# Optimization experiments

Hardware: AMD Instinct MI355X
Metric: run time of the kernel (lower is better)

Reference implementation:

```python
import jax, jax.numpy as jnp
import numpy as np

NUM_Q, NUM_C, E = 12000, 1000, 256
B, S, MC = 32, 200, 4
H = E  # hidden_size == emb_size


def _mlp(x, lin_w, lin_b, out_w, out_b):
    # MLP with n_layer=1: relu(Linear) then output Linear (dropout is identity in eval)
    x = jax.nn.relu(x @ lin_w.T + lin_b)
    return x @ out_w.T + out_b


def _lstm(x, w_ih, w_hh, b_ih, b_hh):
    # torch nn.LSTM(batch_first) semantics, gate order i,f,g,o
    def step(carry, xt):
        h, cs = carry
        gates = xt @ w_ih.T + b_ih + h @ w_hh.T + b_hh
        i, f, g, o = jnp.split(gates, 4, axis=-1)
        cs = jax.nn.sigmoid(f) * cs + jax.nn.sigmoid(i) * jnp.tanh(g)
        h = jax.nn.sigmoid(o) * jnp.tanh(cs)
        return (h, cs), h
    b = x.shape[0]
    init = (jnp.zeros((b, H), x.dtype), jnp.zeros((b, H), x.dtype))
    _, hs = jax.lax.scan(step, init, jnp.swapaxes(x, 0, 1))
    return jnp.swapaxes(hs, 0, 1)


def _avg_fusion_concepts(y_concept, cshft):
    # gather-average over concept ids (equivalent to one_hot*mul*sum in the torch code)
    mask = (cshft != -1)
    idx = jnp.where(mask, cshft, 0)
    gathered = jnp.take_along_axis(y_concept, idx, axis=-1) * mask  # [B,S-1,MC]
    cnt = mask.sum(-1)
    return gathered.sum(-1) / jnp.maximum(cnt, 1)


def _avg_skill_emb(c, concept_emb):
    # QueEmb.get_avg_skill_emb: zero row prepended, -1 padding -> index 0
    cat = jnp.concatenate([jnp.zeros((1, E), concept_emb.dtype), concept_emb], axis=0)
    rc = c + 1
    s = cat[rc].sum(axis=-2)  # [B,S,E]
    n = jnp.maximum((rc != 0).sum(axis=-1), 1)
    return s / n[..., None]


def setup_inputs() -> dict:
    key = jax.random.key(0)
    ks = jax.random.split(key, 24)
    f = jnp.float32
    def lin(k, out_d, in_d):
        bound = 1.0 / np.sqrt(in_d)
        k1, k2 = jax.random.split(k)
        return (jax.random.uniform(k1, (out_d, in_d), f, -bound, bound),
                jax.random.uniform(k2, (out_d,), f, -bound, bound))
    qn_lw, qn_lb = lin(ks[0], 3 * H, 3 * H)
    qn_ow, qn_ob = lin(ks[1], 1, 3 * H)
    cn_lw, cn_lb = lin(ks[2], 3 * H, 3 * H)
    cn_ow, cn_ob = lin(ks[3], NUM_C, 3 * H)
    qa_lw, qa_lb = lin(ks[4], H, H)
    qa_ow, qa_ob = lin(ks[5], NUM_Q, H)
    ca_lw, ca_lb = lin(ks[6], H, H)
    ca_ow, ca_ob = lin(ks[7], NUM_C, H)
    w_ih, b_ih = lin(ks[8], 4 * H, 4 * E)
    w_hh, b_hh = lin(ks[9], 4 * H, H)
    return {
        'q': jax.random.randint(ks[10], (B, S), 0, NUM_Q),
        'c': jax.random.randint(ks[11], (B, S, MC), 0, NUM_C),
        'r': jax.random.randint(ks[12], (B, S), 0, 2),
        'qshft': jax.random.randint(ks[13], (B, S - 1), 0, NUM_Q),
        'cshft': jax.random.randint(ks[14], (B, S - 1, MC), 0, NUM_C),
        'que_emb': jax.random.normal(ks[15], (NUM_Q, E), f) * 0.02,
        'concept_emb': jax.random.normal(ks[16], (NUM_C, E), f) * 0.02,
        'w_ih': w_ih, 'w_hh': w_hh, 'b_ih': b_ih, 'b_hh': b_hh,
        'qn_lw': qn_lw, 'qn_lb': qn_lb, 'qn_ow': qn_ow, 'qn_ob': qn_ob,
        'cn_lw': cn_lw, 'cn_lb': cn_lb, 'cn_ow': cn_ow, 'cn_ob': cn_ob,
        'qa_lw': qa_lw, 'qa_lb': qa_lb, 'qa_ow': qa_ow, 'qa_ob': qa_ob,
        'ca_lw': ca_lw, 'ca_lb': ca_lb, 'ca_ow': ca_ow, 'ca_ob': ca_ob,
    }


def reference(q, c, r, qshft, cshft, que_emb, concept_emb, w_ih, w_hh, b_ih, b_hh,
              qn_lw, qn_lb, qn_ow, qn_ob, cn_lw, cn_lb, cn_ow, cn_ob,
              qa_lw, qa_lb, qa_ow, qa_ob, ca_lw, ca_lb, ca_ow, ca_ob):
    emb_q = que_emb[q]                               # [B,S,E]
    emb_c = _avg_skill_emb(c, concept_emb)           # [B,S,E]
    emb_qc = jnp.concatenate([emb_q, emb_c], -1)     # [B,S,2E]
    rf = r.astype(emb_qc.dtype)[..., None]
    emb_qca = jnp.concatenate([emb_qc * (1 - rf), emb_qc * rf], -1)  # [B,S,4E]

    emb_qc_shift = emb_qc[:, 1:]
    emb_qca_current = emb_qca[:, :-1]
    h = _lstm(emb_qca_current, w_ih, w_hh, b_ih, b_hh)  # [B,S-1,H]  (dropout: eval)
    h_next = jnp.concatenate([emb_qc_shift, h], -1)     # [B,S-1,3H]

    y_question_next = jax.nn.sigmoid(_mlp(h_next, qn_lw, qn_lb, qn_ow, qn_ob)).squeeze(-1)
    y_concept_next = jax.nn.sigmoid(_mlp(h_next, cn_lw, cn_lb, cn_ow, cn_ob))   # [B,S-1,num_c]
    y_question_all = jax.nn.sigmoid(_mlp(h, qa_lw, qa_lb, qa_ow, qa_ob))        # [B,S-1,num_q]
    y_concept_all = jax.nn.sigmoid(_mlp(h, ca_lw, ca_lb, ca_ow, ca_ob))         # [B,S-1,num_c]

    y_concept_next = _avg_fusion_concepts(y_concept_next, cshft)
    y_question_all = jnp.take_along_axis(y_question_all, qshft[..., None], axis=-1).squeeze(-1)
    y_concept_all = _avg_fusion_concepts(y_concept_all, cshft)
    return (y_question_next, y_concept_next, y_question_all, y_concept_all)
```

## Files before the change

### kernel.cpp

```cpp
#include <hip/hip_runtime.h>
#include <hip/hip_bf16.h>

typedef __hip_bfloat16 bf16;
typedef __attribute__((ext_vector_type(8))) short short8;
typedef __attribute__((ext_vector_type(4))) short short4v;
typedef __attribute__((ext_vector_type(4))) float float4v;

#define MFMA16(a,b,c) __builtin_amdgcn_mfma_f32_16x16x32_bf16((a),(b),(c),0,0,0)

#define NB 32
#define NS 200
#define NT 199
#define NBT (NB*NT)
#define HSTR 272

__device__ __forceinline__ float bf2f(bf16 x){ return __bfloat162float(x); }
__device__ __forceinline__ bf16 f2bf(float x){ return __float2bfloat16(x); }
__device__ __forceinline__ float rcp_(float x){ return __builtin_amdgcn_rcpf(x); }
__device__ __forceinline__ float sigmoidf_(float x){ return rcp_(1.0f+__expf(-x)); }
__device__ __forceinline__ float tanhf_(float x){ return 1.0f - 2.0f*rcp_(__expf(2.0f*x)+1.0f); }

union BU { bf16 b; unsigned short u; };
__device__ __forceinline__ unsigned short b2u(bf16 x){ BU t; t.b = x; return t.u; }
__device__ __forceinline__ float u2f(unsigned short x){ BU t; t.u = x; return bf2f(t.b); }

template<typename T>
__device__ __forceinline__ float ldf(const T* p, size_t i){
  if constexpr (sizeof(T) == 4) return p[i]; else return bf2f(p[i]);
}

__device__ __forceinline__ float wave_reduce(float v){
  #pragma unroll
  for (int o=32;o>0;o>>=1) v += __shfl_xor(v, o, 64);
  return v;
}

__device__ __forceinline__ void burn(int iters){
  float x = 1.0f;
  for (int i=0;i<iters;i++)
    x = __builtin_fmaf(x, 1.0000001f, 1.0e-9f);
  asm volatile("" :: "v"(x));
}

__device__ __forceinline__ int poll_xready_rlx(int* xchunk, int lane){
  int tgt = (lane < 25) ? ((lane == 24) ? 7 : 8) : 0;
  int v = 0;
  if (lane < 25)
    v = __hip_atomic_load(&xchunk[lane], __ATOMIC_RELAXED, __HIP_MEMORY_SCOPE_AGENT);
  unsigned long long full = __ballot(v >= tgt);
  unsigned long long notfull = ~full;
  int firstbad = (notfull == 0ULL) ? 64 : (__ffsll((unsigned long long)notfull) - 1);
  int rdy = firstbad * 8;
  return (rdy > NT) ? NT : rdy;
}

__global__ void k_detect(const unsigned short* qe, int* flag){
  int big = 0;
  for (int j = threadIdx.x; j < 128; j += 64){
    int ex = (qe[j] >> 7) & 0xFF;
    if (ex >= 128) big = 1;
  }
  unsigned long long m = __ballot(big);
  if (threadIdx.x == 0) flag[0] = (__popcll(m) >= 2) ? 1 : 0;
}

__global__ void k_sentinel(void* out, int n, float v, const int* flag){
  int i = blockIdx.x*256 + threadIdx.x;
  if (i < n){ if (flag[0]) ((float*)out)[i] = v; else ((bf16*)out)[i] = f2bf(v); }
}

__global__ __launch_bounds__(1024) void k_cvt(
    const void* s0, const void* s1, const void* s2, const void* s3,
    const void* s4, const void* s5, const void* s6, const void* s7,
    bf16* out, const int* flag){
  size_t i = (size_t)blockIdx.x*1024 + threadIdx.x;
  const size_t sz[8] = {1048576,262144,589824,589824,65536,65536,4096,4096};
  const void* sp[8] = {s0,s1,s2,s3,s4,s5,s6,s7};
  size_t off = i; int s = 0;
  while (s < 8 && off >= sz[s]){ off -= sz[s]; s++; }
  if (s >= 8) return;
  if (flag[0]) out[i] = f2bf(((const float*)sp[s])[off]);
  else         out[i] = ((const bf16*)sp[s])[off];
}

template<typename T>
__device__ __forceinline__ void embed_body(const int* q, const int* c,
    const T* que_emb, const T* concept_emb, bf16* emb_qc){
  int p = blockIdx.x;
  int e = threadIdx.x;
  int qi = q[p];
  emb_qc[(size_t)p*512 + e] = f2bf(ldf(que_emb, (size_t)qi*256 + e));
  float s = 0.f; int cnt = 0;
  #pragma unroll
  for (int m=0;m<4;m++){
    int ci = c[p*4+m];
    if (ci >= 0){ cnt++; s += ldf(concept_emb, (size_t)ci*256 + e); }
  }
  s /= (float)(cnt > 0 ? cnt : 1);
  emb_qc[(size_t)p*512 + 256 + e] = f2bf(s);
}
__global__ __launch_bounds__(256) void k_embed(const int* q, const int* c,
    const void* qe, const void* ce, bf16* emb_qc, const int* flag, int* cnt){
  if (blockIdx.x == 0 && threadIdx.x < 32) cnt[threadIdx.x] = 0;
  if (flag[0]) embed_body<float>(q, c, (const float*)qe, (const float*)ce, emb_qc);
  else         embed_body<bf16 >(q, c, (const bf16*)qe,  (const bf16*)ce,  emb_qc);
}

__device__ void gemm_x_unit(int t, int ny, int ltid, unsigned short* xs,
    const bf16* E, const int* r, const bf16* W, const bf16* bc1, const bf16* bc2, bf16* Xp){
  int lane = ltid & 63, wv = ltid >> 6;
  int col = lane & 15, quad = lane >> 4, kq = quad*8;
  const bf16* e0 = E + (size_t)(col*NS + t)*512;
  const bf16* e1 = E + (size_t)((col+16)*NS + t)*512;
  int rv0 = r[col*NS + t], rv1 = r[(col+16)*NS + t];
  int n_base = ny*256 + wv*64;
  const bf16* w0 = W + (size_t)(n_base + col)*1024 + kq;
  short8 z8 = {};
  float4v acc[2][4] = {};
  for (int k0 = 0; k0 < 1024; k0 += 32){
    bool lo = (k0 < 512);
    short8 a0 = *(const short8*)(e0 + (k0 & 511) + kq);
    short8 a1 = *(const short8*)(e1 + (k0 & 511) + kq);
    a0 = (lo == (rv0 == 0)) ? a0 : z8;
    a1 = (lo == (rv1 == 0)) ? a1 : z8;
    short8 bb[4];
    #pragma unroll
    for (int ni=0;ni<4;ni++) bb[ni] = *(const short8*)(w0 + (size_t)ni*16*1024 + k0);
    #pragma unroll
    for (int ni=0;ni<4;ni++){
      acc[0][ni] = MFMA16(a0, bb[ni], acc[0][ni]);
      acc[1][ni] = MFMA16(a1, bb[ni], acc[1][ni]);
    }
  }
  #pragma unroll
  for (int ni=0;ni<4;ni++){
    int n = n_base + ni*16 + col;
    float bs = bf2f(bc1[n]) + bf2f(bc2[n]);
    int nloc = wv*64 + ni*16 + col;
    #pragma unroll
    for (int mi=0;mi<2;mi++)
      #pragma unroll
      for (int reg=0;reg<4;reg++)
        xs[nloc*40 + mi*16 + quad*4 + reg] = b2u(f2bf(acc[mi][ni][reg] + bs));
  }
  __syncthreads();
  int nloc = ltid;
  size_t n = (size_t)ny*256 + nloc;
  short8 v0 = *(const short8*)&xs[nloc*40 + 0];
  short8 v1 = *(const short8*)&xs[nloc*40 + 8];
  short8 v2 = *(const short8*)&xs[nloc*40 + 16];
  short8 v3 = *(const short8*)&xs[nloc*40 + 24];
  bf16* base = Xp + (size_t)t*2*16384 + n*16;
  *(short8*)(base)             = v0;
  *(short8*)(base + 8)         = v1;
  *(short8*)(base + 16384)     = v2;
  *(short8*)(base + 16384 + 8) = v3;
}

__device__ void lstm_role(const bf16* Xp, const bf16* Whh, bf16* Hg,
                          unsigned short* smem, int* cnt){
  int* xchunk = cnt;
  int* hprog  = cnt + 25;
  unsigned short* wlds = smem;
  unsigned short* hbuf = smem + 65536;

  int lane = threadIdx.x & 63, w = threadIdx.x >> 6;
  int col = lane & 15, quad = lane >> 4, kq = quad*8;
  int b0 = blockIdx.x*16;

  for (int i = threadIdx.x; i < 16*HSTR; i += 512) hbuf[i] = 0;

  short8 bfrag[4][8];
  #pragma unroll
  for (int tix=0; tix<4; tix++){
    int g = tix >> 1, ct = tix & 1;
    int nb = g*256 + w*32 + ct*16;
    #pragma unroll
    for (int ks=0; ks<8; ks++)
      bfrag[tix][ks] = *(const volatile short8*)(Whh + (size_t)(nb + col)*256 + ks*32 + kq);
  }
  short8 wofrag[2][8];
  #pragma unroll
  for (int j=0; j<2; j++){
    int nb = 3*256 + w*32 + j*16;
    #pragma unroll
    for (int ks=0; ks<8; ks++)
      wofrag[j][ks] = *(const volatile short8*)(Whh + (size_t)(nb + col)*256 + ks*32 + kq);
  }
  #pragma unroll
  for (int j=0; j<2; j++){
    int nb = 2*256 + w*32 + j*16;
    #pragma unroll
    for (int ks=0; ks<8; ks++){
      short8 v = *(const short8*)(Whh + (size_t)(nb + col)*256 + ks*32 + kq);
      *(short8*)&wlds[(((w*2+j)*8 + ks)*64 + lane)*8] = v;
    }
  }
  __syncthreads();

  float cs[2][4] = {};
  short4v xq[8], xqn[8];

  int ready = 0;
  while (ready < 1){
    int p = poll_xready_rlx(xchunk, lane);
    if (p > ready){
      __builtin_amdgcn_fence(__ATOMIC_ACQUIRE, "agent");
      ready = p;
    } else __builtin_amdgcn_s_sleep(16);
  }
  {
    const bf16* xb = Xp + (size_t)blockIdx.x*16384 + quad*4;
    #pragma unroll
    for (int g=0; g<4; g++)
      #pragma unroll
      for (int ct=0; ct<2; ct++)
        xq[g*2+ct] = *(const short4v*)(xb + (size_t)(g*256 + w*32 + ct*16 + col)*16);
  }

  for (int t=0; t<NT; t++){
    int tn = (t+1 < NT) ? t+1 : t;
    while (ready < tn+1){
      int p = poll_xready_rlx(xchunk, lane);
      if (p > ready){
        __builtin_amdgcn_fence(__ATOMIC_ACQUIRE, "agent");
        ready = p;
      } else __builtin_amdgcn_s_sleep(16);
    }
    const bf16* xbn = Xp + ((size_t)tn*2 + blockIdx.x)*16384 + quad*4;
    #pragma unroll
    for (int g=0; g<4; g++)
      #pragma unroll
      for (int ct=0; ct<2; ct++)
        xqn[g*2+ct] = *(const short4v*)(xbn + (size_t)(g*256 + w*32 + ct*16 + col)*16);

    float4v acc[8];
    #pragma unroll
    for (int j=0; j<8; j++)
      #pragma unroll
      for (int rg=0; rg<4; rg++)
        acc[j][rg] = u2f((unsigned short)xq[j][rg]);

    const unsigned short* hrow = &hbuf[(t&1)*(16*HSTR) + col*HSTR + kq];
    #pragma unroll
    for (int ks=0; ks<8; ks++){
      short8 af = *(const short8*)(hrow + ks*32);
      #pragma unroll
      for (int tix=0; tix<4; tix++) acc[tix] = MFMA16(af, bfrag[tix][ks], acc[tix]);
      #pragma unroll
      for (int j=0; j<2; j++){
        short8 lw = *(const short8*)&wlds[(((w*2+j)*8 + ks)*64 + lane)*8];
        acc[4+j] = MFMA16(af, lw, acc[4+j]);
      }
      acc[6] = MFMA16(af, wofrag[0][ks], acc[6]);
      acc[7] = MFMA16(af, wofrag[1][ks], acc[7]);
    }

    unsigned short* hw = &hbuf[((t+1)&1)*(16*HSTR)];
    #pragma unroll
    for (int ct=0; ct<2; ct++){
      int hc = w*32 + ct*16 + col;
      #pragma unroll
      for (int reg=0; reg<4; reg++){
        float iv = sigmoidf_(acc[0+ct][reg]);
        float fv = sigmoidf_(acc[2+ct][reg]);
        float gv = tanhf_   (acc[4+ct][reg]);
        float ov = sigmoidf_(acc[6+ct][reg]);
        float cc = fv*cs[ct][reg] + iv*gv;
        cs[ct][reg] = cc;
        hw[(quad*4+reg)*HSTR + hc] = b2u(f2bf(ov*tanhf_(cc)));
      }
    }
    #pragma unroll
    for (int i=0;i<8;i++) xq[i] = xqn[i];
    __syncthreads();
    if (((t & 1) == 0) && threadIdx.x == ((((unsigned)t >> 1) & 7) << 6))
      __hip_atomic_store(&hprog[blockIdx.x], t, __ATOMIC_RELEASE, __HIP_MEMORY_SCOPE_AGENT);
    {
      int ri = threadIdx.x >> 5, ci2 = threadIdx.x & 31;
      short8 v = *(const short8*)&hbuf[((t+1)&1)*(16*HSTR) + ri*HSTR + ci2*8];
      *(short8*)(Hg + ((size_t)t*NB + b0 + ri)*256 + ci2*8) = v;
    }
  }
  __syncthreads();
  if (threadIdx.x == 0)
    __hip_atomic_store(&hprog[blockIdx.x], NT, __ATOMIC_RELEASE, __HIP_MEMORY_SCOPE_AGENT);
}

#define HPAD 776
#define SPAD 264
template<typename T>
__device__ void head_pair(int t0, int tid, unsigned short* hsb, unsigned short* hss,
    const bf16* E, const bf16* Hg,
    const bf16* qn_w, const bf16* cn_w, const bf16* qa_w, const bf16* ca_w,
    const T* qn_lb, const T* qn_ow, const T* qn_ob,
    const T* cn_lb, const T* cn_ow, const T* cn_ob,
    const T* qa_lb, const T* qa_ow, const T* qa_ob,
    const T* ca_lb, const T* ca_ow, const T* ca_ob,
    const int* qshft, const int* cshft, void* out, int isf32){
  int hf = tid >> 8, ltid = tid & 255;
  int lane = ltid & 63, wv = ltid >> 6;
  int col = lane & 15, quad = lane >> 4, kq = quad*8;
  const bf16* h0 = Hg + ((size_t)t0*NB + col)*256;
  const bf16* h1 = Hg + ((size_t)t0*NB + col + 16)*256;
  const bf16* e0 = E + ((size_t)col*NS + t0 + 1)*512;
  const bf16* e1 = E + ((size_t)(col+16)*NS + t0 + 1)*512;

  for (int hd=0; hd<2; hd++){
    if (hf == 0){
      const bf16* W = hd ? cn_w : qn_w;
      const T*   Bb = hd ? cn_lb : qn_lb;
      const bf16* wb = W + (size_t)(wv*192 + col)*768 + kq;
      float4v acc[2][12] = {};
      for (int k0 = 0; k0 < 768; k0 += 32){
        short8 a0 = (k0 < 512) ? *(const short8*)(e0 + k0 + kq)
                               : *(const short8*)(h0 + (k0-512) + kq);
        short8 a1 = (k0 < 512) ? *(const short8*)(e1 + k0 + kq)
                               : *(const short8*)(h1 + (k0-512) + kq);
        #pragma unroll
        for (int ni=0; ni<12; ni++){
          short8 bv = *(const short8*)(wb + (size_t)ni*16*768 + k0);
          acc[0][ni] = MFMA16(a0, bv, acc[0][ni]);
          acc[1][ni] = MFMA16(a1, bv, acc[1][ni]);
        }
      }
      #pragma unroll
      for (int ni=0; ni<12; ni++){
        int n = wv*192 + ni*16 + col;
        float bs = ldf(Bb, n);
        #pragma unroll
        for (int mi=0; mi<2; mi++)
          #pragma unroll
          for (int reg=0; reg<4; reg++){
            int rl = mi*16 + quad*4 + reg;
            hsb[rl*HPAD + n] = b2u(f2bf(fmaxf(acc[mi][ni][reg] + bs, 0.0f)));
          }
      }
    } else {
      const bf16* W = hd ? ca_w : qa_w;
      const T*   Bb = hd ? ca_lb : qa_lb;
      const bf16* wb = W + (size_t)(wv*64 + col)*256 + kq;
      float4v acc[2][4] = {};
      for (int k0 = 0; k0 < 256; k0 += 32){
        short8 av0 = *(const short8*)(h0 + k0 + kq);
        short8 av1 = *(const short8*)(h1 + k0 + kq);
        #pragma unroll
        for (int ni=0; ni<4; ni++){
          short8 bv = *(const short8*)(wb + (size_t)ni*16*256 + k0);
          acc[0][ni] = MFMA16(av0, bv, acc[0][ni]);
          acc[1][ni] = MFMA16(av1, bv, acc[1][ni]);
        }
      }
      #pragma unroll
      for (int ni=0; ni<4; ni++){
        int n = wv*64 + ni*16 + col;
        float bs = ldf(Bb, n);
        #pragma unroll
        for (int mi=0; mi<2; mi++)
          #pragma unroll
          for (int reg=0; reg<4; reg++){
            int rl = mi*16 + quad*4 + reg;
            hss[rl*SPAD + n] = b2u(f2bf(fmaxf(acc[mi][ni][reg] + bs, 0.0f)));
          }
      }
    }
    __syncthreads();
    if (hf == 0){
      for (int rr=0; rr<8; rr++){
        int rl = wv*8 + rr, p = rl*NT + t0;
        if (hd == 0){
          float d = 0.f;
          for (int i=lane; i<768; i+=64) d += u2f(hsb[rl*HPAD + i]) * ldf(qn_ow, i);
          d = wave_reduce(d);
          if (lane == 0){
            float v = sigmoidf_(d + ldf(qn_ob, 0));
            if (isf32) ((float*)out)[p] = v; else ((bf16*)out)[p] = f2bf(v);
          }
        } else {
          float sum = 0.f; int cnt = 0;
          #pragma unroll
          for (int m=0; m<4; m++){
            int cid = cshft[p*4+m];
            if (cid >= 0){
              cnt++;
              const T* ww = cn_ow + (size_t)cid*768;
              float d = 0.f;
              for (int i=lane; i<768; i+=64) d += u2f(hsb[rl*HPAD + i]) * ldf(ww, i);
              d = wave_reduce(d);
              sum += sigmoidf_(d + ldf(cn_ob, cid));
            }
          }
          if (lane == 0){
            float v = sum / (float)(cnt > 0 ? cnt : 1);
            if (isf32) ((float*)out)[NBT+p] = v; else ((bf16*)out)[NBT+p] = f2bf(v);
          }
        }
      }
    } else {
      for (int rr=0; rr<8; rr++){
        int rl = wv*8 + rr, p = rl*NT + t0;
        if (hd == 0){
          int qid = qshft[p];
          const T* ww = qa_ow + (size_t)qid*256;
          float d = 0.f;
          for (int i=lane; i<256; i+=64) d += u2f(hss[rl*SPAD + i]) * ldf(ww, i);
          d = wave_reduce(d);
          if (lane == 0){
            float v = sigmoidf_(d + ldf(qa_ob, qid));
            if (isf32) ((float*)out)[2*NBT+p] = v; else ((bf16*)out)[2*NBT+p] = f2bf(v);
          }
        } else {
          float sum = 0.f; int cnt = 0;
          #pragma unroll
          for (int m=0; m<4; m++){
            int cid = cshft[p*4+m];
            if (cid >= 0){
              cnt++;
              const T* ww = ca_ow + (size_t)cid*256;
              float d = 0.f;
              for (int i=lane; i<256; i+=64) d += u2f(hss[rl*SPAD + i]) * ldf(ww, i);
              d = wave_reduce(d);
              sum += sigmoidf_(d + ldf(ca_ob, cid));
            }
          }
          if (lane == 0){
            float v = sum / (float)(cnt > 0 ? cnt : 1);
            if (isf32) ((float*)out)[3*NBT+p] = v; else ((bf16*)out)[3*NBT+p] = f2bf(v);
          }
        }
      }
    }
    __syncthreads();
  }
}

__global__ __launch_bounds__(512)
__attribute__((amdgpu_waves_per_eu(2, 2)))
void k_fused(const bf16* E, const int* r, const bf16* wih, const bf16* bih, const bf16* bhh,
             bf16* Xp, const bf16* whh, bf16* Hg,
             const bf16* qn_w, const bf16* cn_w, const bf16* qa_w, const bf16* ca_w,
             const void* qn_lb, const void* qn_ow, const void* qn_ob,
             const void* cn_lb, const void* cn_ow, const void* cn_ob,
             const void* qa_lb, const void* qa_ow, const void* qa_ob,
             const void* ca_lb, const void* ca_ow, const void* ca_ob,
             const int* qshft, const int* cshft, void* out, const int* flag, int* cnt){
  extern __shared__ __align__(16) unsigned short smem[];
  int* xchunk = cnt;
  int* hprog  = cnt + 25;

  if (blockIdx.x < 2){
    lstm_role(Xp, whh, Hg, smem, cnt);
    return;
  }
  if ((blockIdx.x & 7) < 2){
    for (;;){
      int a = __hip_atomic_load(&hprog[0], __ATOMIC_RELAXED, __HIP_MEMORY_SCOPE_AGENT);
      int b = __hip_atomic_load(&hprog[1], __ATOMIC_RELAXED, __HIP_MEMORY_SCOPE_AGENT);
      if (a >= NT && b >= NT) break;
      burn(2048);
    }
    return;
  }

  int tid = threadIdx.x, hf = tid >> 8, ltid = tid & 255;
  int rank = blockIdx.x - 2*(blockIdx.x >> 3) - 2;
  int t1 = rank;
  int t2 = (rank < 49) ? rank + 150 : -1;
  volatile int* lflag = (volatile int*)(smem + 73728);

  for (int ti = 0; ti < 2; ti++){
    int t = (ti == 0) ? t1 : t2;
    if (t < 0) break;
    unsigned short* xs = smem + hf*(256*40);
    gemm_x_unit(t, hf,     ltid, xs, E, r, wih, bih, bhh, Xp);
    __syncthreads();
    gemm_x_unit(t, 2 + hf, ltid, xs, E, r, wih, bih, bhh, Xp);
    __syncthreads();
    if (tid == 0)
      __hip_atomic_fetch_add(&xchunk[t >> 3], 1, __ATOMIC_RELEASE, __HIP_MEMORY_SCOPE_AGENT);
  }

  unsigned short* hsb = smem;
  unsigned short* hss = smem + 32*HPAD;
  for (int ti = 0; ti < 2; ti++){
    int t0 = (ti == 0) ? t1 : t2;
    if (t0 < 0) break;
    if (tid == 0) *lflag = 0;
    __syncthreads();
    {
      int need = t0 + 1;
      for (;;){
        if (tid == 0){
          int a = __hip_atomic_load(&hprog[0], __ATOMIC_RELAXED, __HIP_MEMORY_SCOPE_AGENT);
          int b = __hip_atomic_load(&hprog[1], __ATOMIC_RELAXED, __HIP_MEMORY_SCOPE_AGENT);
          if (a >= need && b >= need){
            __builtin_amdgcn_fence(__ATOMIC_ACQUIRE, "agent");
            *lflag = 1;
          }
        }
        if (*lflag) break;
        burn(256);
      }
    }
    __syncthreads();

    if (flag[0])
      head_pair<float>(t0, tid, hsb, hss, E, Hg, qn_w, cn_w, qa_w, ca_w,
        (const float*)qn_lb, (const float*)qn_ow, (const float*)qn_ob,
        (const float*)cn_lb, (const float*)cn_ow, (const float*)cn_ob,
        (const float*)qa_lb, (const float*)qa_ow, (const float*)qa_ob,
        (const float*)ca_lb, (const float*)ca_ow, (const float*)ca_ob,
        qshft, cshft, out, 1);
    else
      head_pair<bf16>(t0, tid, hsb, hss, E, Hg, qn_w, cn_w, qa_w, ca_w,
        (const bf16*)qn_lb, (const bf16*)qn_ow, (const bf16*)qn_ob,
        (const bf16*)cn_lb, (const bf16*)cn_ow, (const bf16*)cn_ob,
        (const bf16*)qa_lb, (const bf16*)qa_ow, (const bf16*)qa_ob,
        (const bf16*)ca_lb, (const bf16*)ca_ow, (const bf16*)ca_ob,
        qshft, cshft, out, 0);
  }

  for (;;){
    int a = __hip_atomic_load(&hprog[0], __ATOMIC_RELAXED, __HIP_MEMORY_SCOPE_AGENT);
    int b = __hip_atomic_load(&hprog[1], __ATOMIC_RELAXED, __HIP_MEMORY_SCOPE_AGENT);
    if (a >= NT && b >= NT) break;
    burn(2048);
  }
}

extern "C" void kernel_launch(void* const* d_in, const int* in_sizes, int n_in,
                              void* d_out, int out_size, void* d_ws, size_t ws_size,
                              hipStream_t stream){
  const int*  q     = (const int*) d_in[0];
  const int*  c     = (const int*) d_in[1];
  const int*  r     = (const int*) d_in[2];
  const int*  qshft = (const int*) d_in[3];
  const int*  cshft = (const int*) d_in[4];
  const void* que_emb  = d_in[5];
  const void* conc_emb = d_in[6];
  const void* w_ih  = d_in[7];
  const void* w_hh  = d_in[8];
  const void* b_ih  = d_in[9];
  const void* b_hh  = d_in[10];
  const void* qn_lw = d_in[11];
  const void* qn_lb = d_in[12];
  const void* qn_ow = d_in[13];
  const void* qn_ob = d_in[14];
  const void* cn_lw = d_in[15];
  const void* cn_lb = d_in[16];
  const void* cn_ow = d_in[17];
  const void* cn_ob = d_in[18];
  const void* qa_lw = d_in[19];
  const void* qa_lb = d_in[20];
  const void* qa_ow = d_in[21];
  const void* qa_ob = d_in[22];
  const void* ca_lw = d_in[23];
  const void* ca_lb = d_in[24];
  const void* ca_ow = d_in[25];
  const void* ca_ob = d_in[26];

  const size_t OFF_FLAG = 0;
  const size_t OFF_EMB  = 256;
  const size_t OFF_XPT  = OFF_EMB + 6553600;
  const size_t OFF_HG   = OFF_XPT + 13041664;
  const size_t OFF_WC   = OFF_HG + 3260416;
  const size_t NEED     = OFF_WC + 5259264;

  char* ws = (char*)d_ws;
  int* flag = (int*)(ws + OFF_FLAG);
  int* cnt  = (int*)(ws + 64);

  k_detect<<<1, 64, 0, stream>>>((const unsigned short*)que_emb, flag);

  if (ws_size < NEED){
    k_sentinel<<<(out_size + 255)/256, 256, 0, stream>>>(d_out, out_size,
        (float)(ws_size >> 20), flag);
    return;
  }

  bf16* emb_qc = (bf16*)(ws + OFF_EMB);
  bf16* Xp     = (bf16*)(ws + OFF_XPT);
  bf16* Hg     = (bf16*)(ws + OFF_HG);
  bf16* Wc     = (bf16*)(ws + OFF_WC);
  bf16* wih_c  = Wc;
  bf16* whh_c  = Wc + 1048576;
  bf16* qnlw_c = Wc + 1310720;
  bf16* cnlw_c = Wc + 1900544;
  bf16* qalw_c = Wc + 2490368;
  bf16* calw_c = Wc + 2555904;
  bf16* bih_c  = Wc + 2621440;
  bf16* bhh_c  = Wc + 2625536;

  hipFuncSetAttribute((const void*)k_fused,
      hipFuncAttributeMaxDynamicSharedMemorySize, 148480);

  k_cvt<<<2568, 1024, 0, stream>>>(w_ih, w_hh, qn_lw, cn_lw, qa_lw, ca_lw,
      b_ih, b_hh, Wc, flag);
  k_embed<<<NB*NS, 256, 0, stream>>>(q, c, que_emb, conc_emb, emb_qc, flag, cnt);
  k_fused<<<201, 512, 148480, stream>>>(emb_qc, r, wih_c, bih_c, bhh_c, Xp, whh_c, Hg,
      qnlw_c, cnlw_c, qalw_c, calw_c,
      qn_lb, qn_ow, qn_ob, cn_lb, cn_ow, cn_ob,
      qa_lb, qa_ow, qa_ob, ca_lb, ca_ow, ca_ob,
      qshft, cshft, d_out, flag, cnt);
}
```

Before: 1.007 ms.

## Assign one timestep per block and replace burn-loop polling with s_sleep

Removes the earlier scheme where some blocks only spun as placeholders and each working block handled up to two timesteps. Now every non-LSTM block handles exactly one timestep: it computes its input-projection chunk, then waits on the LSTM progress counters using s_sleep instead of an FMA burn loop, then runs the output heads. The intent is to stop wasting CU issue slots on busy-wait ALU work and to spread head work across more blocks. This depends on the host launching one block per timestep, which is in the unseen launch code. If that launch grid was not updated, the change risks coverage gaps or co-residency deadlock, since blocks spin while waiting on other blocks.

```diff
diff --git a/kernel.cpp b/kernel.cpp
--- a/kernel.cpp
+++ b/kernel.cpp
@@ -33,13 +33,6 @@
   #pragma unroll
   for (int o=32;o>0;o>>=1) v += __shfl_xor(v, o, 64);
   return v;
-}
-
-__device__ __forceinline__ void burn(int iters){
-  float x = 1.0f;
-  for (int i=0;i<iters;i++)
-    x = __builtin_fmaf(x, 1.0000001f, 1.0e-9f);
-  asm volatile("" :: "v"(x));
 }
 
 __device__ __forceinline__ int poll_xready_rlx(int* xchunk, int lane){
@@ -452,80 +445,55 @@
     lstm_role(Xp, whh, Hg, smem, cnt);
     return;
   }
-  if ((blockIdx.x & 7) < 2){
-    for (;;){
-      int a = __hip_atomic_load(&hprog[0], __ATOMIC_RELAXED, __HIP_MEMORY_SCOPE_AGENT);
-      int b = __hip_atomic_load(&hprog[1], __ATOMIC_RELAXED, __HIP_MEMORY_SCOPE_AGENT);
-      if (a >= NT && b >= NT) break;
-      burn(2048);
-    }
-    return;
-  }
-
+
+  int t0  = blockIdx.x - 2;
   int tid = threadIdx.x, hf = tid >> 8, ltid = tid & 255;
-  int rank = blockIdx.x - 2*(blockIdx.x >> 3) - 2;
-  int t1 = rank;
-  int t2 = (rank < 49) ? rank + 150 : -1;
   volatile int* lflag = (volatile int*)(smem + 73728);
 
-  for (int ti = 0; ti < 2; ti++){
-    int t = (ti == 0) ? t1 : t2;
-    if (t < 0) break;
+  {
     unsigned short* xs = smem + hf*(256*40);
-    gemm_x_unit(t, hf,     ltid, xs, E, r, wih, bih, bhh, Xp);
+    gemm_x_unit(t0, hf,     ltid, xs, E, r, wih, bih, bhh, Xp);
     __syncthreads();
-    gemm_x_unit(t, 2 + hf, ltid, xs, E, r, wih, bih, bhh, Xp);
+    gemm_x_unit(t0, 2 + hf, ltid, xs, E, r, wih, bih, bhh, Xp);
+    if (tid == 0) *lflag = 0;
     __syncthreads();
     if (tid == 0)
-      __hip_atomic_fetch_add(&xchunk[t >> 3], 1, __ATOMIC_RELEASE, __HIP_MEMORY_SCOPE_AGENT);
-  }
+      __hip_atomic_fetch_add(&xchunk[t0 >> 3], 1, __ATOMIC_RELEASE, __HIP_MEMORY_SCOPE_AGENT);
+  }
+
+  {
+    int need = t0 + 1;
+    for (;;){
+      if (tid == 0){
+        int a = __hip_atomic_load(&hprog[0], __ATOMIC_RELAXED, __HIP_MEMORY_SCOPE_AGENT);
+        int b = __hip_atomic_load(&hprog[1], __ATOMIC_RELAXED, __HIP_MEMORY_SCOPE_AGENT);
+        if (a >= need && b >= need){
+          __builtin_amdgcn_fence(__ATOMIC_ACQUIRE, "agent");
+          *lflag = 1;
+        }
+      }
+      if (*lflag) break;
+      __builtin_amdgcn_s_sleep(32);
+    }
+  }
+  __syncthreads();
 
   unsigned short* hsb = smem;
   unsigned short* hss = smem + 32*HPAD;
-  for (int ti = 0; ti < 2; ti++){
-    int t0 = (ti == 0) ? t1 : t2;
-    if (t0 < 0) break;
-    if (tid == 0) *lflag = 0;
-    __syncthreads();
-    {
-      int need = t0 + 1;
-      for (;;){
-        if (tid == 0){
-          int a = __hip_atomic_load(&hprog[0], __ATOMIC_RELAXED, __HIP_MEMORY_SCOPE_AGENT);
-          int b = __hip_atomic_load(&hprog[1], __ATOMIC_RELAXED, __HIP_MEMORY_SCOPE_AGENT);
-          if (a >= need && b >= need){
-            __builtin_amdgcn_fence(__ATOMIC_ACQUIRE, "agent");
-            *lflag = 1;
-          }
-        }
-        if (*lflag) break;
-        burn(256);
-      }
-    }
-    __syncthreads();
-
-    if (flag[0])
-      head_pair<float>(t0, tid, hsb, hss, E, Hg, qn_w, cn_w, qa_w, ca_w,
-        (const float*)qn_lb, (const float*)qn_ow, (const float*)qn_ob,
-        (const float*)cn_lb, (const float*)cn_ow, (const float*)cn_ob,
-        (const float*)qa_lb, (const float*)qa_ow, (const float*)qa_ob,
-        (const float*)ca_lb, (const float*)ca_ow, (const float*)ca_ob,
-        qshft, cshft, out, 1);
-    else
-      head_pair<bf16>(t0, tid, hsb, hss, E, Hg, qn_w, cn_w, qa_w, ca_w,
-        (const bf16*)qn_lb, (const bf16*)qn_ow, (const bf16*)qn_ob,
-        (const bf16*)cn_lb, (const bf16*)cn_ow, (const bf16*)cn_ob,
-        (const bf16*)qa_lb, (const bf16*)qa_ow, (const bf16*)qa_ob,
-        (const bf16*)ca_lb, (const bf16*)ca_ow, (const bf16*)ca_ob,
-        qshft, cshft, out, 0);
-  }
-
-  for (;;){
-    int a = __hip_atomic_load(&hprog[0], __ATOMIC_RELAXED, __HIP_MEMORY_SCOPE_AGENT);
-    int b = __hip_atomic_load(&hprog[1], __ATOMIC_RELAXED, __HIP_MEMORY_SCOPE_AGENT);
-    if (a >= NT && b >= NT) break;
-    burn(2048);
-  }
+  if (flag[0])
+    head_pair<float>(t0, tid, hsb, hss, E, Hg, qn_w, cn_w, qa_w, ca_w,
+      (const float*)qn_lb, (const float*)qn_ow, (const float*)qn_ob,
+      (const float*)cn_lb, (const float*)cn_ow, (const float*)cn_ob,
+      (const float*)qa_lb, (const float*)qa_ow, (const float*)qa_ob,
+      (const float*)ca_lb, (const float*)ca_ow, (const float*)ca_ob,
+      qshft, cshft, out, 1);
+  else
+    head_pair<bf16>(t0, tid, hsb, hss, E, Hg, qn_w, cn_w, qa_w, ca_w,
+      (const bf16*)qn_lb, (const bf16*)qn_ow, (const bf16*)qn_ob,
+      (const bf16*)cn_lb, (const bf16*)cn_ow, (const bf16*)cn_ob,
+      (const bf16*)qa_lb, (const bf16*)qa_ow, (const bf16*)qa_ob,
+      (const bf16*)ca_lb, (const bf16*)ca_ow, (const bf16*)ca_ob,
+      qshft, cshft, out, 0);
 }
 
 extern "C" void kernel_launch(void* const* d_in, const int* in_sizes, int n_in,
```

Measured after the change: 1.013 ms. No clear change (+0.6%).
